# Kernel tuning notes

Measured on AMD Instinct MI355X. Metric: run time of the kernel, lower is better.

The kernel has to match this reference:

```python
import jax, jax.numpy as jnp
import numpy as np

N_TRIAL = 1_000_000
N_STIM = 10_000
N_DIM = 16
N_GROUP = 4
N_REF = 8  # row = 1 query + 8 references
BETA = 1.0
GAMMA = 0.001
N_SELECT = np.array([1, 2, 3, 1], dtype=np.int32)  # per-config n_select (config_list)


def setup_inputs() -> dict:
    key = jax.random.key(0)
    k1, k2, k3, k4, k5 = jax.random.split(key, 5)
    stimulus_set = jax.random.randint(k1, (N_TRIAL, N_REF + 1), 0, N_STIM, dtype=jnp.int64)
    config_idx = jax.random.randint(k2, (N_TRIAL,), 0, len(N_SELECT), dtype=jnp.int64)
    group_id = jax.random.randint(k3, (N_TRIAL,), 0, N_GROUP, dtype=jnp.int64)
    is_present = jnp.ones((N_TRIAL, N_REF + 1), dtype=jnp.int32)
    embed_z = jax.random.normal(k4, (N_STIM, N_DIM), dtype=jnp.float32)
    attention_w = jax.random.uniform(k5, (N_GROUP, N_DIM), dtype=jnp.float32)
    return {
        "stimulus_set": stimulus_set,
        "config_idx": config_idx,
        "group_id": group_id,
        "is_present": is_present,
        "embed_z": embed_z,
        "attention_w": attention_w,
    }


def reference(stimulus_set, config_idx, group_id, is_present, embed_z, attention_w):
    # coordinate: embedding lookup -> (T, R+1, D)
    z = embed_z[stimulus_set]
    z_q = z[:, :1, :]   # (T, 1, D)
    z_r = z[:, 1:, :]   # (T, R, D)
    # attention: per-group dimension weights -> (T, 1, D)
    w = attention_w[group_id][:, None, :]
    # kernel: attention-weighted Minkowski (rho=2) distance + exponential similarity
    d = jnp.sqrt(jnp.sum(w * (z_q - z_r) ** 2, axis=-1))  # (T, R)
    sim_qr = jnp.exp(-BETA * d) + GAMMA
    # mask absent references (is_present[:, 1:])
    sim_qr = sim_qr * is_present[:, 1:].astype(sim_qr.dtype)
    # Ranked-sequence (Luce choice) probability, vectorized over all configs:
    # seq_prob = prod_{j < n_select} sim[:, j] / sum_{i >= j} sim[:, i]
    suffix = jnp.cumsum(sim_qr[:, ::-1], axis=1)[:, ::-1]  # (T, R) suffix sums
    n_select = jnp.asarray(N_SELECT)[config_idx]           # (T,)
    mask = jnp.arange(N_REF)[None, :] < n_select[:, None]  # (T, R)
    denom = jnp.where(mask, suffix, 1.0)
    prob = jnp.where(mask, sim_qr / denom, 1.0)
    likelihood = jnp.prod(prob, axis=1)  # (T,)
    return likelihood
```

## Files before the change

### kernel.cpp

```cpp
#include <hip/hip_runtime.h>
#include <math.h>

#define N_TRIAL 1000000
#define N_REF 8
#define N_DIM 16
#define N_GROUP 4
#define BETA 1.0f
#define GAMMA 0.001f
#define N_SELECT_PACKED 0x1321

typedef float v4f __attribute__((ext_vector_type(4)));

#define WAVES_PER_BLOCK 4
#define ROW_STRIDE 72

__global__ __launch_bounds__(256, 4) void likelihood_kernel(
    const int* __restrict__ stim,
    const int* __restrict__ config,
    const int* __restrict__ group,
    const int* __restrict__ present,
    const float* __restrict__ embed,
    const float* __restrict__ attw,
    float* __restrict__ out)
{
    __shared__ float d2buf[WAVES_PER_BLOCK][N_REF][ROW_STRIDE];

    const int tid  = threadIdx.x;
    const int wv   = tid >> 6;
    const int lane = tid & 63;
    const int q    = lane >> 2;
    const int s    = lane & 3;

    const int wtb = blockIdx.x * 256 + wv * 64;

    const float* embed_s = embed + s * 4;

    float* row_a = &d2buf[wv][2 * s][0];
    float* row_b = &d2buf[wv][2 * s + 1][0];

    for (int j = 0; j < 4; ++j) {
        int t  = wtb + 16 * j + q;
        int tc = (t < N_TRIAL) ? t : (N_TRIAL - 1);

        const int* sp = stim + tc * (N_REF + 1);
        const int* pp = present + tc * (N_REF + 1);

        int idx[N_REF + 1];
#pragma unroll
        for (int i = 0; i <= N_REF; ++i) idx[i] = sp[i];

        int pr[N_REF];
#pragma unroll
        for (int r = 0; r < N_REF; ++r) pr[r] = pp[1 + r];

        int g = group[tc];
        v4f w  = *(const v4f*)(attw + g * N_DIM + s * 4);
        v4f zq = *(const v4f*)(embed_s + idx[0] * N_DIM);

#pragma unroll
        for (int r = 0; r < N_REF; ++r) {
            v4f zr = *(const v4f*)(embed_s + idx[1 + r] * N_DIM);
            v4f dd = zq - zr;
            v4f p  = w * dd * dd;
            float d2 = (p.x + p.y) + (p.z + p.w);
            d2 += __shfl_xor(d2, 1);
            d2 += __shfl_xor(d2, 2);
            d2 = (pr[r] != 0) ? d2 : -1.0f;
            if (r == 2 * s)     row_a[16 * j + q] = d2;
            if (r == 2 * s + 1) row_b[16 * j + q] = d2;
        }
    }

    __syncthreads();

    int t2  = wtb + lane;
    int t2c = (t2 < N_TRIAL) ? t2 : (N_TRIAL - 1);

    float sim[N_REF];
#pragma unroll
    for (int r = 0; r < N_REF; ++r) {
        float d2 = d2buf[wv][r][lane];
        float e  = __expf(-BETA * sqrtf(d2)) + GAMMA;
        sim[r] = (d2 < 0.0f) ? 0.0f : e;
    }

    int c  = config[t2c];
    int ns = (N_SELECT_PACKED >> ((c & 3) * 4)) & 0xF;

    float suf2 = sim[7];
#pragma unroll
    for (int r = 6; r >= 2; --r) suf2 += sim[r];
    float suf1 = suf2 + sim[1];
    float suf0 = suf1 + sim[0];

    float num = sim[0] * ((ns >= 2) ? sim[1] : 1.0f) * ((ns >= 3) ? sim[2] : 1.0f);
    float den = suf0   * ((ns >= 2) ? suf1   : 1.0f) * ((ns >= 3) ? suf2   : 1.0f);

    if (t2 < N_TRIAL)
        out[t2] = __fdividef(num, den);
}

extern "C" void kernel_launch(void* const* d_in, const int* in_sizes, int n_in,
                              void* d_out, int out_size, void* d_ws, size_t ws_size,
                              hipStream_t stream) {
    const int*   stim    = (const int*)d_in[0];
    const int*   config  = (const int*)d_in[1];
    const int*   group   = (const int*)d_in[2];
    const int*   present = (const int*)d_in[3];
    const float* embed   = (const float*)d_in[4];
    const float* attw    = (const float*)d_in[5];
    float*       out     = (float*)d_out;

    int blocks = (N_TRIAL + 255) / 256;
    likelihood_kernel<<<blocks, 256, 0, stream>>>(stim, config, group, present,
                                                  embed, attw, out);
}
```

Measured before the change: 159.4 us.

## Stage stimulus indices through LDS with coalesced loads and drop block barrier

Each wave now copies its 64 trials' stimulus rows into shared memory with contiguous int4 loads. The four-way redundant per-lane strided loads of indices are replaced by LDS reads. Presence flags, config and group are loaded once per lane, with presence as vector loads and group distributed via shuffle. The presence mask becomes a multiply. The block-wide __syncthreads is removed, relying on intra-wave LDS ordering, and the occupancy hint in launch_bounds is dropped. The edge wave is clamped to the last full window. The risks are an ordering hazard from the missing barrier and higher register use.

```diff
diff --git a/kernel.cpp b/kernel.cpp
--- a/kernel.cpp
+++ b/kernel.cpp
@@ -9,12 +9,13 @@
 #define GAMMA 0.001f
 #define N_SELECT_PACKED 0x1321
 
-typedef float v4f __attribute__((ext_vector_type(4)));
+#define WPB 4
+#define D2_STRIDE 72
 
-#define WAVES_PER_BLOCK 4
-#define ROW_STRIDE 72
+typedef float v4f  __attribute__((ext_vector_type(4)));
+typedef int   v4iu __attribute__((ext_vector_type(4), aligned(4)));
 
-__global__ __launch_bounds__(256, 4) void likelihood_kernel(
+__global__ __launch_bounds__(256) void likelihood_kernel(
     const int* __restrict__ stim,
     const int* __restrict__ config,
     const int* __restrict__ group,
@@ -23,7 +24,8 @@
     const float* __restrict__ attw,
     float* __restrict__ out)
 {
-    __shared__ float d2buf[WAVES_PER_BLOCK][N_REF][ROW_STRIDE];
+    __shared__ int4  s_stim4[WPB][144];
+    __shared__ float s_d2[WPB][N_REF][D2_STRIDE];
 
     const int tid  = threadIdx.x;
     const int wv   = tid >> 6;
@@ -31,60 +33,62 @@
     const int q    = lane >> 2;
     const int s    = lane & 3;
 
-    const int wtb = blockIdx.x * 256 + wv * 64;
+    int wtb = blockIdx.x * 256 + wv * 64;
+    const bool valid = (wtb + lane) < N_TRIAL;
+    if (wtb > N_TRIAL - 64) wtb = N_TRIAL - 64;
+
+    {
+        const int4* g4 = (const int4*)(stim + wtb * 9);
+        s_stim4[wv][lane]      = g4[lane];
+        s_stim4[wv][64 + lane] = g4[64 + lane];
+        if (lane < 16) s_stim4[wv][128 + lane] = g4[128 + lane];
+    }
+
+    const int t2 = wtb + lane;
+    const int* pp = present + t2 * 9;
+    v4iu p0 = *(const v4iu*)(pp + 1);
+    v4iu p1 = *(const v4iu*)(pp + 5);
+    int  c    = config[t2];
+    int  gall = group[t2];
 
     const float* embed_s = embed + s * 4;
 
-    float* row_a = &d2buf[wv][2 * s][0];
-    float* row_b = &d2buf[wv][2 * s + 1][0];
+    for (int j = 0; j < 4; ++j) {
+        const int* sp = (const int*)&s_stim4[wv][0] + (16 * j + q) * 9;
+        int idx[9];
+#pragma unroll
+        for (int i = 0; i < 9; ++i) idx[i] = sp[i];
 
-    for (int j = 0; j < 4; ++j) {
-        int t  = wtb + 16 * j + q;
-        int tc = (t < N_TRIAL) ? t : (N_TRIAL - 1);
-
-        const int* sp = stim + tc * (N_REF + 1);
-        const int* pp = present + tc * (N_REF + 1);
-
-        int idx[N_REF + 1];
-#pragma unroll
-        for (int i = 0; i <= N_REF; ++i) idx[i] = sp[i];
-
-        int pr[N_REF];
-#pragma unroll
-        for (int r = 0; r < N_REF; ++r) pr[r] = pp[1 + r];
-
-        int g = group[tc];
+        int g  = __shfl(gall, 16 * j + q);
         v4f w  = *(const v4f*)(attw + g * N_DIM + s * 4);
         v4f zq = *(const v4f*)(embed_s + idx[0] * N_DIM);
 
+        float d2v[N_REF];
 #pragma unroll
         for (int r = 0; r < N_REF; ++r) {
             v4f zr = *(const v4f*)(embed_s + idx[1 + r] * N_DIM);
             v4f dd = zq - zr;
-            v4f p  = w * dd * dd;
-            float d2 = (p.x + p.y) + (p.z + p.w);
+            v4f wd = w * dd;
+            float d2 = (wd.x * dd.x + wd.y * dd.y) + (wd.z * dd.z + wd.w * dd.w);
             d2 += __shfl_xor(d2, 1);
             d2 += __shfl_xor(d2, 2);
-            d2 = (pr[r] != 0) ? d2 : -1.0f;
-            if (r == 2 * s)     row_a[16 * j + q] = d2;
-            if (r == 2 * s + 1) row_b[16 * j + q] = d2;
+            d2v[r] = d2;
         }
+        float da = (s == 0) ? d2v[0] : (s == 1) ? d2v[2] : (s == 2) ? d2v[4] : d2v[6];
+        float db = (s == 0) ? d2v[1] : (s == 1) ? d2v[3] : (s == 2) ? d2v[5] : d2v[7];
+        s_d2[wv][2 * s    ][16 * j + q] = da;
+        s_d2[wv][2 * s + 1][16 * j + q] = db;
     }
 
-    __syncthreads();
-
-    int t2  = wtb + lane;
-    int t2c = (t2 < N_TRIAL) ? t2 : (N_TRIAL - 1);
+    int pr[N_REF] = {p0.x, p0.y, p0.z, p0.w, p1.x, p1.y, p1.z, p1.w};
 
     float sim[N_REF];
 #pragma unroll
     for (int r = 0; r < N_REF; ++r) {
-        float d2 = d2buf[wv][r][lane];
-        float e  = __expf(-BETA * sqrtf(d2)) + GAMMA;
-        sim[r] = (d2 < 0.0f) ? 0.0f : e;
+        float d2 = s_d2[wv][r][lane];
+        sim[r] = (__expf(-BETA * sqrtf(d2)) + GAMMA) * (float)pr[r];
     }
 
-    int c  = config[t2c];
     int ns = (N_SELECT_PACKED >> ((c & 3) * 4)) & 0xF;
 
     float suf2 = sim[7];
@@ -96,8 +100,8 @@
     float num = sim[0] * ((ns >= 2) ? sim[1] : 1.0f) * ((ns >= 3) ? sim[2] : 1.0f);
     float den = suf0   * ((ns >= 2) ? suf1   : 1.0f) * ((ns >= 3) ? suf2   : 1.0f);
 
-    if (t2 < N_TRIAL)
-        out[t2] = __fdividef(num, den);
+    if (valid)
+        out[wtb + lane] = __fdividef(num, den);
 }
 
 extern "C" void kernel_launch(void* const* d_in, const int* in_sizes, int n_in,
```

Measured after the change: 139.8 us. -12.3%, faster.
